# Kernel tuning notes

Hardware: AMD Instinct MI355X
Metric: run time of the kernel (lower is better)

## Reference

```python
import jax, jax.numpy as jnp
import numpy as np

B = 65536
N_WORKER, N_PROJECT, EMB = 1807, 2490, 10
STATE_DIM = 2 * EMB          # 20
HIDDEN = 2 * STATE_DIM       # 40
ACTION_DIM = EMB             # 10


def setup_inputs() -> dict:
    key = jax.random.key(0)
    ks = jax.random.split(key, 8)
    worker_ids = jax.random.randint(ks[0], (B,), 0, N_WORKER)
    project_ids = jax.random.randint(ks[1], (B,), 0, N_PROJECT)
    worker_emb = jax.random.normal(ks[2], (N_WORKER, EMB), dtype=jnp.float32)
    project_emb = jax.random.normal(ks[3], (N_PROJECT, EMB), dtype=jnp.float32)
    W1 = jax.random.normal(ks[4], (HIDDEN, STATE_DIM), dtype=jnp.float32) / np.sqrt(STATE_DIM)
    b1 = jnp.zeros((HIDDEN,), dtype=jnp.float32)
    W2 = jax.random.normal(ks[5], (ACTION_DIM, HIDDEN), dtype=jnp.float32) / np.sqrt(HIDDEN)
    b2 = jnp.zeros((ACTION_DIM,), dtype=jnp.float32)
    return {"worker_ids": worker_ids, "project_ids": project_ids,
            "worker_emb": worker_emb, "project_emb": project_emb,
            "W1": W1, "b1": b1, "W2": W2, "b2": b2}


def reference(worker_ids, project_ids, worker_emb, project_emb, W1, b1, W2, b2):
    we = worker_emb[worker_ids]              # [B, 10]
    pe = project_emb[project_ids]            # [B, 10]
    x = jnp.concatenate([we, pe], axis=-1)   # [B, 20]
    h = jax.nn.relu(x @ W1.T + b1)           # [B, 40]
    the_weights = (h @ W2.T + b2)[:, None, :]  # [B, 1, 10]
    # original loop rebuilds rows 1..2489 of the project table -> single slice
    table = project_emb[1:N_PROJECT]         # [2489, 10]
    p = jnp.einsum('bqd,nd->bqn', the_weights, table)  # [B, 1, 2489]
    argmax = jnp.argmax(p, axis=2)           # [B, 1]
    return argmax + 1
```

## Files before the change

### kernel.cpp

```cpp
#include <hip/hip_runtime.h>
#include <float.h>

using v2f = __attribute__((ext_vector_type(2))) float;
using v4f = __attribute__((ext_vector_type(4))) float;

#define EMB 10
#define STATE 20
#define HIDDEN 40
#define NPROJ 2490

__device__ __forceinline__ void score_pair(const v4f* __restrict__ tbl4, int p,
                                           const v2f wv2[5],
                                           float& best, int& bidx) {
    const v4f* tp = tbl4 + p * 5;
    v4f a0 = tp[0], a1 = tp[1], a2 = tp[2], a3 = tp[3], a4 = tp[4];
    v2f c0 = wv2[0] * a0.lo;
    c0 += wv2[1] * a0.hi; c0 += wv2[2] * a1.lo;
    c0 += wv2[3] * a1.hi; c0 += wv2[4] * a2.lo;
    float s0 = c0.x + c0.y;
    v2f c1 = wv2[0] * a2.hi;
    c1 += wv2[1] * a3.lo; c1 += wv2[2] * a3.hi;
    c1 += wv2[3] * a4.lo; c1 += wv2[4] * a4.hi;
    float s1 = c1.x + c1.y;
    float sp = s0; int ip = 2 * p;
    if (s1 > sp) { sp = s1; ip = 2 * p + 1; }
    if (sp > best) { best = sp; bidx = ip; }
}

__global__ __launch_bounds__(256, 2) void actor_kernel(
    const int* __restrict__ wid, const int* __restrict__ pid,
    const float* __restrict__ wemb, const float* __restrict__ pemb,
    const float* __restrict__ W1, const float* __restrict__ b1,
    const float* __restrict__ W2, const float* __restrict__ b2,
    int* __restrict__ out)
{
    __shared__ float sb[4][64];
    __shared__ int   si[4][64];

    const int tid  = threadIdx.x;
    const int lane = tid & 63;
    const int wave = tid >> 6;
    const int g    = wave >> 1;
    const int h    = wave & 1;
    const int b    = blockIdx.x * 128 + g * 64 + lane;

    const v4f* __restrict__ tbl4 =
        (const v4f*)__builtin_assume_aligned(pemb, 16);

    const int wi = wid[b];
    const int pi = pid[b];
    const float* __restrict__ wr = wemb + wi * EMB;
    const float* __restrict__ pr = pemb + pi * EMB;
    v2f x2[STATE / 2];
    #pragma unroll
    for (int k = 0; k < EMB / 2; ++k) x2[k] = *(const v2f*)(wr + 2 * k);
    #pragma unroll
    for (int k = 0; k < EMB / 2; ++k) x2[EMB / 2 + k] = *(const v2f*)(pr + 2 * k);

    float hb[HIDDEN];
    #pragma unroll 4
    for (int j = 0; j < HIDDEN; ++j) {
        const v2f* w1r = (const v2f*)(W1 + j * STATE);
        v2f a = w1r[0] * x2[0];
        #pragma unroll
        for (int k = 1; k < STATE / 2; ++k) a += w1r[k] * x2[k];
        hb[j] = fmaxf(a.x + a.y + b1[j], 0.0f);
    }
    v2f h2[HIDDEN / 2];
    #pragma unroll
    for (int k = 0; k < HIDDEN / 2; ++k) h2[k] = (v2f){hb[2 * k], hb[2 * k + 1]};

    v2f wv2[5];
    #pragma unroll
    for (int d = 0; d < EMB; d += 2) {
        const v2f* w2r0 = (const v2f*)(W2 + d * HIDDEN);
        const v2f* w2r1 = (const v2f*)(W2 + (d + 1) * HIDDEN);
        v2f a0 = w2r0[0] * h2[0];
        v2f a1 = w2r1[0] * h2[0];
        #pragma unroll
        for (int k = 1; k < HIDDEN / 2; ++k) { a0 += w2r0[k] * h2[k]; a1 += w2r1[k] * h2[k]; }
        wv2[d / 2] = (v2f){a0.x + a0.y + b2[d], a1.x + a1.y + b2[d + 1]};
    }

    float best = -FLT_MAX;
    int   bidx = 1;

    if (h == 0) {
        {
            v2f c0v = *(const v2f*)(pemb + 10);
            v4f c1v = *(const v4f*)(pemb + 12);
            v4f c2v = *(const v4f*)(pemb + 16);
            v2f a = wv2[0] * c0v;
            a += wv2[1] * c1v.lo; a += wv2[2] * c1v.hi;
            a += wv2[3] * c2v.lo; a += wv2[4] * c2v.hi;
            best = a.x + a.y; bidx = 1;
        }
        #pragma unroll 4
        for (int p = 1; p < 623; ++p) score_pair(tbl4, p, wv2, best, bidx);
    } else {
        #pragma unroll 4
        for (int p = 623; p < 1245; ++p) score_pair(tbl4, p, wv2, best, bidx);
    }

    sb[wave][lane] = best;
    si[wave][lane] = bidx;
    __syncthreads();
    if (h == 0) {
        float v  = sb[wave + 1][lane];
        int   vi = si[wave + 1][lane];
        if (v > best) { best = v; bidx = vi; }
        out[b] = bidx;
    }
}

extern "C" void kernel_launch(void* const* d_in, const int* in_sizes, int n_in,
                              void* d_out, int out_size, void* d_ws, size_t ws_size,
                              hipStream_t stream) {
    const int*   wid  = (const int*)  d_in[0];
    const int*   pid  = (const int*)  d_in[1];
    const float* wemb = (const float*)d_in[2];
    const float* pemb = (const float*)d_in[3];
    const float* W1   = (const float*)d_in[4];
    const float* b1   = (const float*)d_in[5];
    const float* W2   = (const float*)d_in[6];
    const float* b2   = (const float*)d_in[7];
    int* out = (int*)d_out;

    const int B = in_sizes[0];
    actor_kernel<<<B / 128, 256, 0, stream>>>(wid, pid, wemb, pemb, W1, b1, W2, b2, out);
}
```

Baseline: 137.1 us.

## Score two batch rows per thread to reuse each table load

Each thread now computes MLP outputs for two batch elements and scores both against every loaded table pair. The table range is split into four chunks across the four waves instead of two, so each table load feeds twice the arithmetic. This cuts table load traffic per score by half. In exchange, every thread runs the MLP twice, which is redundant across the four waves, and register pressure goes up.

```diff
diff --git a/kernel.cpp b/kernel.cpp
--- a/kernel.cpp
+++ b/kernel.cpp
@@ -8,49 +8,14 @@
 #define STATE 20
 #define HIDDEN 40
 #define NPROJ 2490
+#define NSPLIT 4
 
-__device__ __forceinline__ void score_pair(const v4f* __restrict__ tbl4, int p,
-                                           const v2f wv2[5],
-                                           float& best, int& bidx) {
-    const v4f* tp = tbl4 + p * 5;
-    v4f a0 = tp[0], a1 = tp[1], a2 = tp[2], a3 = tp[3], a4 = tp[4];
-    v2f c0 = wv2[0] * a0.lo;
-    c0 += wv2[1] * a0.hi; c0 += wv2[2] * a1.lo;
-    c0 += wv2[3] * a1.hi; c0 += wv2[4] * a2.lo;
-    float s0 = c0.x + c0.y;
-    v2f c1 = wv2[0] * a2.hi;
-    c1 += wv2[1] * a3.lo; c1 += wv2[2] * a3.hi;
-    c1 += wv2[3] * a4.lo; c1 += wv2[4] * a4.hi;
-    float s1 = c1.x + c1.y;
-    float sp = s0; int ip = 2 * p;
-    if (s1 > sp) { sp = s1; ip = 2 * p + 1; }
-    if (sp > best) { best = sp; bidx = ip; }
-}
-
-__global__ __launch_bounds__(256, 2) void actor_kernel(
-    const int* __restrict__ wid, const int* __restrict__ pid,
-    const float* __restrict__ wemb, const float* __restrict__ pemb,
+__device__ __forceinline__ void mlp_eval(
+    const float* __restrict__ wr, const float* __restrict__ pr,
     const float* __restrict__ W1, const float* __restrict__ b1,
     const float* __restrict__ W2, const float* __restrict__ b2,
-    int* __restrict__ out)
+    v2f wv2[5])
 {
-    __shared__ float sb[4][64];
-    __shared__ int   si[4][64];
-
-    const int tid  = threadIdx.x;
-    const int lane = tid & 63;
-    const int wave = tid >> 6;
-    const int g    = wave >> 1;
-    const int h    = wave & 1;
-    const int b    = blockIdx.x * 128 + g * 64 + lane;
-
-    const v4f* __restrict__ tbl4 =
-        (const v4f*)__builtin_assume_aligned(pemb, 16);
-
-    const int wi = wid[b];
-    const int pi = pid[b];
-    const float* __restrict__ wr = wemb + wi * EMB;
-    const float* __restrict__ pr = pemb + pi * EMB;
     v2f x2[STATE / 2];
     #pragma unroll
     for (int k = 0; k < EMB / 2; ++k) x2[k] = *(const v2f*)(wr + 2 * k);
@@ -70,7 +35,6 @@
     #pragma unroll
     for (int k = 0; k < HIDDEN / 2; ++k) h2[k] = (v2f){hb[2 * k], hb[2 * k + 1]};
 
-    v2f wv2[5];
     #pragma unroll
     for (int d = 0; d < EMB; d += 2) {
         const v2f* w2r0 = (const v2f*)(W2 + d * HIDDEN);
@@ -81,35 +45,95 @@
         for (int k = 1; k < HIDDEN / 2; ++k) { a0 += w2r0[k] * h2[k]; a1 += w2r1[k] * h2[k]; }
         wv2[d / 2] = (v2f){a0.x + a0.y + b2[d], a1.x + a1.y + b2[d + 1]};
     }
+}
 
-    float best = -FLT_MAX;
-    int   bidx = 1;
+__device__ __forceinline__ float dot_row(const float* __restrict__ row, const v2f wv[5]) {
+    v2f c0 = *(const v2f*)(row + 0);
+    v4f c1 = *(const v4f*)(row + 2);
+    v4f c2 = *(const v4f*)(row + 6);
+    v2f a = wv[0] * c0;
+    a += wv[1] * c1.lo; a += wv[2] * c1.hi;
+    a += wv[3] * c2.lo; a += wv[4] * c2.hi;
+    return a.x + a.y;
+}
 
+__device__ __forceinline__ void score_pair2(const v4f* __restrict__ tbl4, int p,
+                                            const v2f wva[5], const v2f wvb[5],
+                                            float& ba, int& ia, float& bb, int& ib) {
+    const v4f* tp = tbl4 + p * 5;
+    v4f a0 = tp[0], a1 = tp[1], a2 = tp[2], a3 = tp[3], a4 = tp[4];
+    v2f c0 = wva[0] * a0.lo;
+    c0 += wva[1] * a0.hi; c0 += wva[2] * a1.lo;
+    c0 += wva[3] * a1.hi; c0 += wva[4] * a2.lo;
+    float s0 = c0.x + c0.y;
+    v2f c1 = wva[0] * a2.hi;
+    c1 += wva[1] * a3.lo; c1 += wva[2] * a3.hi;
+    c1 += wva[3] * a4.lo; c1 += wva[4] * a4.hi;
+    float s1 = c1.x + c1.y;
+    float sp = s0; int ip = 2 * p;
+    if (s1 > sp) { sp = s1; ip = 2 * p + 1; }
+    if (sp > ba) { ba = sp; ia = ip; }
+    v2f d0 = wvb[0] * a0.lo;
+    d0 += wvb[1] * a0.hi; d0 += wvb[2] * a1.lo;
+    d0 += wvb[3] * a1.hi; d0 += wvb[4] * a2.lo;
+    float t0 = d0.x + d0.y;
+    v2f d1 = wvb[0] * a2.hi;
+    d1 += wvb[1] * a3.lo; d1 += wvb[2] * a3.hi;
+    d1 += wvb[3] * a4.lo; d1 += wvb[4] * a4.hi;
+    float t1 = d1.x + d1.y;
+    float tp2 = t0; int jp = 2 * p;
+    if (t1 > tp2) { tp2 = t1; jp = 2 * p + 1; }
+    if (tp2 > bb) { bb = tp2; ib = jp; }
+}
+
+__global__ __launch_bounds__(256, 2) void actor_kernel(
+    const int* __restrict__ wid, const int* __restrict__ pid,
+    const float* __restrict__ wemb, const float* __restrict__ pemb,
+    const float* __restrict__ W1, const float* __restrict__ b1,
+    const float* __restrict__ W2, const float* __restrict__ b2,
+    int* __restrict__ out)
+{
+    __shared__ float sb[NSPLIT][2][64];
+    __shared__ int   si[NSPLIT][2][64];
+
+    const int tid  = threadIdx.x;
+    const int lane = tid & 63;
+    const int h    = tid >> 6;
+    const int b0   = blockIdx.x * 128 + lane;
+    const int b1i  = b0 + 64;
+
+    const v4f* __restrict__ tbl4 = (const v4f*)__builtin_assume_aligned(pemb, 16);
+
+    v2f wva[5], wvb[5];
+    mlp_eval(wemb + wid[b0] * EMB, pemb + pid[b0] * EMB, W1, b1, W2, b2, wva);
+    mlp_eval(wemb + wid[b1i] * EMB, pemb + pid[b1i] * EMB, W1, b1, W2, b2, wvb);
+
+    float ba = -FLT_MAX, bb = -FLT_MAX;
+    int   ia = 1, ib = 1;
+
+    const int plo[NSPLIT + 1] = {1, 312, 623, 934, 1245};
     if (h == 0) {
-        {
-            v2f c0v = *(const v2f*)(pemb + 10);
-            v4f c1v = *(const v4f*)(pemb + 12);
-            v4f c2v = *(const v4f*)(pemb + 16);
-            v2f a = wv2[0] * c0v;
-            a += wv2[1] * c1v.lo; a += wv2[2] * c1v.hi;
-            a += wv2[3] * c2v.lo; a += wv2[4] * c2v.hi;
-            best = a.x + a.y; bidx = 1;
-        }
-        #pragma unroll 4
-        for (int p = 1; p < 623; ++p) score_pair(tbl4, p, wv2, best, bidx);
-    } else {
-        #pragma unroll 4
-        for (int p = 623; p < 1245; ++p) score_pair(tbl4, p, wv2, best, bidx);
+        ba = dot_row(pemb + 10, wva); ia = 1;
+        bb = dot_row(pemb + 10, wvb); ib = 1;
     }
+    const int lo = plo[h], hi = plo[h + 1];
+    #pragma unroll 4
+    for (int p = lo; p < hi; ++p)
+        score_pair2(tbl4, p, wva, wvb, ba, ia, bb, ib);
 
-    sb[wave][lane] = best;
-    si[wave][lane] = bidx;
+    sb[h][0][lane] = ba; si[h][0][lane] = ia;
+    sb[h][1][lane] = bb; si[h][1][lane] = ib;
     __syncthreads();
     if (h == 0) {
-        float v  = sb[wave + 1][lane];
-        int   vi = si[wave + 1][lane];
-        if (v > best) { best = v; bidx = vi; }
-        out[b] = bidx;
+        #pragma unroll
+        for (int k = 1; k < NSPLIT; ++k) {
+            float v0 = sb[k][0][lane]; int j0 = si[k][0][lane];
+            if (v0 > ba) { ba = v0; ia = j0; }
+            float v1 = sb[k][1][lane]; int j1 = si[k][1][lane];
+            if (v1 > bb) { bb = v1; ib = j1; }
+        }
+        out[b0]  = ia;
+        out[b1i] = ib;
     }
 }
 
```

New measurement: 177.3 us. 29.4% more time.

## Split the project-table scan across four waves per row group

Applied to the files above, without the earlier changes.

Each block now handles 64 batch rows with four waves, each scanning a quarter of the project table, instead of two waves per group over 128 rows. Every wave recomputes the small MLP for its rows, trading redundant arithmetic for twice as many blocks and more waves per CU to hide load latency. The partial argmax results are merged in shared memory across four slices, and launch bounds request higher occupancy.

```diff
diff --git a/kernel.cpp b/kernel.cpp
--- a/kernel.cpp
+++ b/kernel.cpp
@@ -8,6 +8,54 @@
 #define STATE 20
 #define HIDDEN 40
 #define NPROJ 2490
+#define NSPLIT 4
+
+__device__ __forceinline__ void mlp_eval(
+    const float* __restrict__ wr, const float* __restrict__ pr,
+    const float* __restrict__ W1, const float* __restrict__ b1,
+    const float* __restrict__ W2, const float* __restrict__ b2,
+    v2f wv2[5])
+{
+    v2f x2[STATE / 2];
+    #pragma unroll
+    for (int k = 0; k < EMB / 2; ++k) x2[k] = *(const v2f*)(wr + 2 * k);
+    #pragma unroll
+    for (int k = 0; k < EMB / 2; ++k) x2[EMB / 2 + k] = *(const v2f*)(pr + 2 * k);
+
+    float hb[HIDDEN];
+    #pragma unroll 4
+    for (int j = 0; j < HIDDEN; ++j) {
+        const v2f* w1r = (const v2f*)(W1 + j * STATE);
+        v2f a = w1r[0] * x2[0];
+        #pragma unroll
+        for (int k = 1; k < STATE / 2; ++k) a += w1r[k] * x2[k];
+        hb[j] = fmaxf(a.x + a.y + b1[j], 0.0f);
+    }
+    v2f h2[HIDDEN / 2];
+    #pragma unroll
+    for (int k = 0; k < HIDDEN / 2; ++k) h2[k] = (v2f){hb[2 * k], hb[2 * k + 1]};
+
+    #pragma unroll
+    for (int d = 0; d < EMB; d += 2) {
+        const v2f* w2r0 = (const v2f*)(W2 + d * HIDDEN);
+        const v2f* w2r1 = (const v2f*)(W2 + (d + 1) * HIDDEN);
+        v2f a0 = w2r0[0] * h2[0];
+        v2f a1 = w2r1[0] * h2[0];
+        #pragma unroll
+        for (int k = 1; k < HIDDEN / 2; ++k) { a0 += w2r0[k] * h2[k]; a1 += w2r1[k] * h2[k]; }
+        wv2[d / 2] = (v2f){a0.x + a0.y + b2[d], a1.x + a1.y + b2[d + 1]};
+    }
+}
+
+__device__ __forceinline__ float dot_row(const float* __restrict__ row, const v2f wv[5]) {
+    v2f c0 = *(const v2f*)(row + 0);
+    v4f c1 = *(const v4f*)(row + 2);
+    v4f c2 = *(const v4f*)(row + 6);
+    v2f a = wv[0] * c0;
+    a += wv[1] * c1.lo; a += wv[2] * c1.hi;
+    a += wv[3] * c2.lo; a += wv[4] * c2.hi;
+    return a.x + a.y;
+}
 
 __device__ __forceinline__ void score_pair(const v4f* __restrict__ tbl4, int p,
                                            const v2f wv2[5],
@@ -27,88 +75,45 @@
     if (sp > best) { best = sp; bidx = ip; }
 }
 
-__global__ __launch_bounds__(256, 2) void actor_kernel(
+__global__ __launch_bounds__(256, 4) void actor_kernel(
     const int* __restrict__ wid, const int* __restrict__ pid,
     const float* __restrict__ wemb, const float* __restrict__ pemb,
     const float* __restrict__ W1, const float* __restrict__ b1,
     const float* __restrict__ W2, const float* __restrict__ b2,
     int* __restrict__ out)
 {
-    __shared__ float sb[4][64];
-    __shared__ int   si[4][64];
+    __shared__ float sb[NSPLIT][64];
+    __shared__ int   si[NSPLIT][64];
 
     const int tid  = threadIdx.x;
     const int lane = tid & 63;
-    const int wave = tid >> 6;
-    const int g    = wave >> 1;
-    const int h    = wave & 1;
-    const int b    = blockIdx.x * 128 + g * 64 + lane;
+    const int h    = tid >> 6;
+    const int b    = blockIdx.x * 64 + lane;
 
-    const v4f* __restrict__ tbl4 =
-        (const v4f*)__builtin_assume_aligned(pemb, 16);
-
-    const int wi = wid[b];
-    const int pi = pid[b];
-    const float* __restrict__ wr = wemb + wi * EMB;
-    const float* __restrict__ pr = pemb + pi * EMB;
-    v2f x2[STATE / 2];
-    #pragma unroll
-    for (int k = 0; k < EMB / 2; ++k) x2[k] = *(const v2f*)(wr + 2 * k);
-    #pragma unroll
-    for (int k = 0; k < EMB / 2; ++k) x2[EMB / 2 + k] = *(const v2f*)(pr + 2 * k);
-
-    float hb[HIDDEN];
-    #pragma unroll 4
-    for (int j = 0; j < HIDDEN; ++j) {
-        const v2f* w1r = (const v2f*)(W1 + j * STATE);
-        v2f a = w1r[0] * x2[0];
-        #pragma unroll
-        for (int k = 1; k < STATE / 2; ++k) a += w1r[k] * x2[k];
-        hb[j] = fmaxf(a.x + a.y + b1[j], 0.0f);
-    }
-    v2f h2[HIDDEN / 2];
-    #pragma unroll
-    for (int k = 0; k < HIDDEN / 2; ++k) h2[k] = (v2f){hb[2 * k], hb[2 * k + 1]};
+    const v4f* __restrict__ tbl4 = (const v4f*)__builtin_assume_aligned(pemb, 16);
 
     v2f wv2[5];
-    #pragma unroll
-    for (int d = 0; d < EMB; d += 2) {
-        const v2f* w2r0 = (const v2f*)(W2 + d * HIDDEN);
-        const v2f* w2r1 = (const v2f*)(W2 + (d + 1) * HIDDEN);
-        v2f a0 = w2r0[0] * h2[0];
-        v2f a1 = w2r1[0] * h2[0];
-        #pragma unroll
-        for (int k = 1; k < HIDDEN / 2; ++k) { a0 += w2r0[k] * h2[k]; a1 += w2r1[k] * h2[k]; }
-        wv2[d / 2] = (v2f){a0.x + a0.y + b2[d], a1.x + a1.y + b2[d + 1]};
-    }
+    mlp_eval(wemb + wid[b] * EMB, pemb + pid[b] * EMB, W1, b1, W2, b2, wv2);
 
     float best = -FLT_MAX;
     int   bidx = 1;
 
-    if (h == 0) {
-        {
-            v2f c0v = *(const v2f*)(pemb + 10);
-            v4f c1v = *(const v4f*)(pemb + 12);
-            v4f c2v = *(const v4f*)(pemb + 16);
-            v2f a = wv2[0] * c0v;
-            a += wv2[1] * c1v.lo; a += wv2[2] * c1v.hi;
-            a += wv2[3] * c2v.lo; a += wv2[4] * c2v.hi;
-            best = a.x + a.y; bidx = 1;
-        }
-        #pragma unroll 4
-        for (int p = 1; p < 623; ++p) score_pair(tbl4, p, wv2, best, bidx);
-    } else {
-        #pragma unroll 4
-        for (int p = 623; p < 1245; ++p) score_pair(tbl4, p, wv2, best, bidx);
-    }
+    const int plo[NSPLIT + 1] = {1, 312, 623, 934, 1245};
+    if (h == 0) { best = dot_row(pemb + 10, wv2); bidx = 1; }
+    const int lo = plo[h], hi = plo[h + 1];
+    #pragma unroll 4
+    for (int p = lo; p < hi; ++p)
+        score_pair(tbl4, p, wv2, best, bidx);
 
-    sb[wave][lane] = best;
-    si[wave][lane] = bidx;
+    sb[h][lane] = best;
+    si[h][lane] = bidx;
     __syncthreads();
     if (h == 0) {
-        float v  = sb[wave + 1][lane];
-        int   vi = si[wave + 1][lane];
-        if (v > best) { best = v; bidx = vi; }
+        #pragma unroll
+        for (int k = 1; k < NSPLIT; ++k) {
+            float v = sb[k][lane]; int j = si[k][lane];
+            if (v > best) { best = v; bidx = j; }
+        }
         out[b] = bidx;
     }
 }
@@ -127,5 +132,5 @@
     int* out = (int*)d_out;
 
     const int B = in_sizes[0];
-    actor_kernel<<<B / 128, 256, 0, stream>>>(wid, pid, wemb, pemb, W1, b1, W2, b2, out);
+    actor_kernel<<<B / 64, 256, 0, stream>>>(wid, pid, wemb, pemb, W1, b1, W2, b2, out);
 }
```

New measurement: 266.7 us. 1.95x slower.
